# Kernel optimization log

Hardware: AMD Instinct MI355X
Metric: run time of the kernel (lower is better)

## Reference

```python
import jax, jax.numpy as jnp
import numpy as np

HIDDEN = 4096
NUM_HEADS = 32
NUM_KV_HEADS = 8
HEAD_DIM = 128
ROPE_THETA = 10000.0


def setup_inputs() -> dict:
    key = jax.random.key(0)
    ks = jax.random.split(key, 5)
    B, N = 2, 2048
    s = 0.02
    return {
        "hidden_states": jax.random.normal(ks[0], (B, N, HIDDEN), dtype=jnp.float32),
        "positions": jnp.tile(jnp.arange(N, dtype=jnp.int32)[None, :], (B, 1)),
        "Wq": jax.random.normal(ks[1], (HIDDEN, NUM_HEADS * HEAD_DIM), dtype=jnp.float32) * s,
        "Wk": jax.random.normal(ks[2], (HIDDEN, NUM_KV_HEADS * HEAD_DIM), dtype=jnp.float32) * s,
        "Wv": jax.random.normal(ks[3], (HIDDEN, NUM_KV_HEADS * HEAD_DIM), dtype=jnp.float32) * s,
        "Wo": jax.random.normal(ks[4], (NUM_HEADS * HEAD_DIM, HIDDEN), dtype=jnp.float32) * s,
    }


def _rotate_half(x):
    half = x.shape[-1] // 2
    return jnp.concatenate([-x[..., half:], x[..., :half]], axis=-1)


def reference(hidden_states, positions, Wq, Wk, Wv, Wo):
    B, N, _ = hidden_states.shape
    H, KVH, D = NUM_HEADS, NUM_KV_HEADS, HEAD_DIM
    rep = H // KVH

    # projections
    q = (hidden_states @ Wq).reshape(B, N, H, D).transpose(0, 2, 1, 3)     # [B,H,N,D]
    k = (hidden_states @ Wk).reshape(B, N, KVH, D).transpose(0, 2, 1, 3)   # [B,KVH,N,D]
    v = (hidden_states @ Wv).reshape(B, N, KVH, D).transpose(0, 2, 1, 3)   # [B,KVH,N,D]

    # rotary embedding
    inv_freq = 1.0 / (ROPE_THETA ** (jnp.arange(0, D, 2, dtype=jnp.float32) / D))
    freqs = positions.astype(jnp.float32)[..., None] * inv_freq            # [B,N,D/2]
    emb = jnp.concatenate([freqs, freqs], axis=-1)                          # [B,N,D]
    cos = jnp.cos(emb)[:, None, :, :]                                       # [B,1,N,D]
    sin = jnp.sin(emb)[:, None, :, :]
    q = q * cos + _rotate_half(q) * sin
    k = k * cos + _rotate_half(k) * sin

    # GQA attention without materializing repeated k/v:
    # group q heads by kv head (repeat_interleave => q head h uses kv group h//rep)
    qg = q.reshape(B, KVH, rep, N, D)
    scale = 1.0 / jnp.sqrt(jnp.asarray(D, dtype=q.dtype))
    scores = jnp.einsum('bgrnd,bgmd->bgrnm', qg, k) * scale                 # [B,KVH,rep,N,N]
    causal = jnp.tril(jnp.ones((N, N), dtype=bool))
    scores = jnp.where(causal, scores, jnp.finfo(scores.dtype).min)
    attn = jax.nn.softmax(scores, axis=-1)
    out = jnp.einsum('bgrnm,bgmd->bgrnd', attn, v)                          # [B,KVH,rep,N,D]
    out = out.reshape(B, H, N, D).transpose(0, 2, 1, 3).reshape(B, N, H * D)
    return out @ Wo
```

## Files before the change

### kernel.cpp

```cpp
#include <hip/hip_runtime.h>
#include <hip/hip_bf16.h>

typedef __bf16 bf16_t;
typedef float  f32x4  __attribute__((ext_vector_type(4)));
typedef bf16_t bf16x4 __attribute__((ext_vector_type(4)));
typedef bf16_t bf16x8 __attribute__((ext_vector_type(8)));

#define MFMA16(a, b, c) __builtin_amdgcn_mfma_f32_16x16x32_bf16((a), (b), (c), 0, 0, 0)

#define GLOAD_LDS16(g, l)                                                              \
  __builtin_amdgcn_global_load_lds((const __attribute__((address_space(1))) void*)(g), \
                                   (__attribute__((address_space(3))) void*)(l), 16, 0, 0)

#define BARRIER    __builtin_amdgcn_s_barrier()
#define WAIT_LGKM0 asm volatile("s_waitcnt lgkmcnt(0)" ::: "memory")
#define WAIT_VM4   asm volatile("s_waitcnt vmcnt(4)" ::: "memory")
#define WAIT_VM6   asm volatile("s_waitcnt vmcnt(6)" ::: "memory")
#define WAIT_VM0   asm volatile("s_waitcnt vmcnt(0)" ::: "memory")

__global__ __launch_bounds__(256) void cvt_bf16(const float* __restrict__ in,
                                                bf16_t* __restrict__ out, int n4) {
  int stride = gridDim.x * blockDim.x;
  for (int i = blockIdx.x * blockDim.x + threadIdx.x; i < n4; i += stride) {
    f32x4 v = ((const f32x4*)in)[i];
    bf16x4 o;
#pragma unroll
    for (int j = 0; j < 4; ++j) o[j] = (bf16_t)v[j];
    ((bf16x4*)out)[i] = o;
  }
}

__global__ __launch_bounds__(256) void transpose_cvt(const float* __restrict__ in,
                                                     bf16_t* __restrict__ out,
                                                     int R, int C) {
  __shared__ float t[64][65];
  int tr0 = blockIdx.y * 64, tc0 = blockIdx.x * 64;
  int tx = threadIdx.x & 15, ty = threadIdx.x >> 4;
#pragma unroll
  for (int i = 0; i < 4; ++i) {
    f32x4 v = *(const f32x4*)(in + (size_t)(tr0 + ty + 16 * i) * C + tc0 + tx * 4);
#pragma unroll
    for (int j = 0; j < 4; ++j) t[ty + 16 * i][tx * 4 + j] = v[j];
  }
  __syncthreads();
#pragma unroll
  for (int i = 0; i < 4; ++i) {
    bf16x4 o4;
#pragma unroll
    for (int j = 0; j < 4; ++j) o4[j] = (bf16_t)t[tx * 4 + j][ty + 16 * i];
    *(bf16x4*)(out + (size_t)(tc0 + ty + 16 * i) * R + tr0 + tx * 4) = o4;
  }
}

#define LDA(buf)                                                                          \
  {                                                                                       \
    const int sb_ = (((buf)*2 + (wr >> 1)) * 128 + (wr & 1) * 64) * 64;                   \
    _Pragma("unroll") for (int mf = 0; mf < 4; ++mf) {                                    \
      int row_ = mf * 16 + ci;                                                            \
      _Pragma("unroll") for (int ks = 0; ks < 2; ++ks)                                    \
          a[mf][ks] = *(const bf16x8*)&lds[sb_ + row_ * 64 +                              \
                                           ((ks * 32 + g * 8) ^ ((ci & 7) << 3))];       \
    }                                                                                     \
  }

#define LDB(buf, nf0, arr)                                                                \
  {                                                                                       \
    const int sb_ = 32768 + ((buf)*2 + wc) * 8192;                                        \
    _Pragma("unroll") for (int j = 0; j < 2; ++j) {                                       \
      int row_ = ((nf0) + j) * 16 + ci;                                                   \
      _Pragma("unroll") for (int ks = 0; ks < 2; ++ks)                                    \
          arr[j][ks] = *(const bf16x8*)&lds[sb_ + row_ * 64 +                             \
                                            ((ks * 32 + g * 8) ^ ((ci & 7) << 3))];      \
    }                                                                                     \
  }

#define MM(arr, NFP)                                                                      \
  {                                                                                       \
    __builtin_amdgcn_s_setprio(1);                                                        \
    _Pragma("unroll") for (int mf = 0; mf < 4; ++mf)                                      \
        _Pragma("unroll") for (int j = 0; j < 2; ++j)                                     \
            _Pragma("unroll") for (int ks = 0; ks < 2; ++ks)                              \
                acc[mf][(NFP) + j] =                                                      \
        MFMA16(a[mf][ks], arr[j][ks], acc[mf][(NFP) + j]);                                \
    __builtin_amdgcn_s_setprio(0);                                                        \
  }

template <int WRITE_BF16>
__global__ __launch_bounds__(512) void gemm8(const bf16_t* __restrict__ A,
                                             const bf16_t* __restrict__ Bt,
                                             void* __restrict__ Cv,
                                             int M, int N, int K, int ntn) {
  __shared__ alignas(16) bf16_t lds[65536];
  (void)M;
  const int tid = threadIdx.x;
  const int lane = tid & 63, w = tid >> 6;
  const int wr = w >> 1, wc = w & 1;
  const int g = lane >> 4, ci = lane & 15;
  const int cpx = gridDim.x >> 3;
  const int wg = ((int)blockIdx.x & 7) * cpx + ((int)blockIdx.x >> 3);
  const int m0 = (wg / ntn) * 256, n0 = (wg % ntn) * 256;
  const int ksw = ((lane & 7) ^ (lane >> 3)) << 3;

  auto stage = [&](const bf16_t* src, int ldsbase) {
#pragma unroll
    for (int j = 0; j < 2; ++j)
      GLOAD_LDS16(src + (size_t)(j * 64 + w * 8 + (lane >> 3)) * K + ksw,
                  (char*)&lds[ldsbase + (j * 64 + w * 8) * 64]);
  };

  bf16x8 a[4][2], b0[2][2], b1[2][2];
  f32x4 acc[4][8];
#pragma unroll
  for (int mf = 0; mf < 4; ++mf)
#pragma unroll
    for (int nf = 0; nf < 8; ++nf) acc[mf][nf] = f32x4{0.f, 0.f, 0.f, 0.f};

  stage(A + (size_t)m0 * K, 0);
  stage(A + (size_t)(m0 + 128) * K, 8192);
  stage(Bt + (size_t)n0 * K, 32768);
  stage(Bt + (size_t)(n0 + 128) * K, 40960);
  WAIT_VM4;
  stage(A + (size_t)m0 * K + 64, 16384);
  stage(A + (size_t)(m0 + 128) * K + 64, 24576);
  stage(Bt + (size_t)n0 * K + 64, 49152);
  WAIT_VM6;
  BARRIER;

  const int NT2 = K >> 7;
  for (int i = 0; i < NT2; ++i) {
    const int keb = i << 7;
    int e2 = keb + 128;
    if (e2 > K - 64) e2 = K - 64;
    int o2 = keb + 192;
    if (o2 > K - 64) o2 = K - 64;
    LDA(0) LDB(0, 0, b0) LDB(0, 2, b1)
    stage(Bt + (size_t)(n0 + 128) * K + keb + 64, 57344);
    BARRIER; WAIT_LGKM0;
    MM(b0, 0)
    BARRIER;
    LDB(0, 4, b0)
    stage(A + (size_t)m0 * K + e2, 0);
    BARRIER; WAIT_LGKM0;
    MM(b1, 2)
    BARRIER;
    LDB(0, 6, b1)
    stage(A + (size_t)(m0 + 128) * K + e2, 8192);
    BARRIER; WAIT_LGKM0;
    MM(b0, 4)
    BARRIER;
    stage(Bt + (size_t)n0 * K + e2, 32768);
    BARRIER; WAIT_LGKM0;
    MM(b1, 6)
    WAIT_VM6;
    BARRIER;
    LDA(1) LDB(1, 0, b0) LDB(1, 2, b1)
    stage(Bt + (size_t)(n0 + 128) * K + e2, 40960);
    BARRIER; WAIT_LGKM0;
    MM(b0, 0)
    BARRIER;
    LDB(1, 4, b0)
    stage(A + (size_t)m0 * K + o2, 16384);
    BARRIER; WAIT_LGKM0;
    MM(b1, 2)
    BARRIER;
    LDB(1, 6, b1)
    stage(A + (size_t)(m0 + 128) * K + o2, 24576);
    BARRIER; WAIT_LGKM0;
    MM(b0, 4)
    BARRIER;
    stage(Bt + (size_t)n0 * K + o2, 49152);
    BARRIER; WAIT_LGKM0;
    MM(b1, 6)
    WAIT_VM6;
    BARRIER;
  }
  WAIT_VM0;

#pragma unroll
  for (int mf = 0; mf < 4; ++mf) {
#pragma unroll
    for (int nf = 0; nf < 8; ++nf) {
      int grow = m0 + wr * 64 + mf * 16 + g * 4;
      int gcol = n0 + wc * 128 + nf * 16 + ci;
#pragma unroll
      for (int r = 0; r < 4; ++r) {
        if (WRITE_BF16)
          ((bf16_t*)Cv)[(size_t)(grow + r) * N + gcol] = (bf16_t)acc[mf][nf][r];
        else
          ((float*)Cv)[(size_t)(grow + r) * N + gcol] = acc[mf][nf][r];
      }
    }
  }
}

__global__ __launch_bounds__(256) void rope_pack(const bf16_t* __restrict__ QKV,
                                                 const int* __restrict__ pos,
                                                 bf16_t* __restrict__ Qr,
                                                 bf16_t* __restrict__ Kr,
                                                 bf16_t* __restrict__ Vr) {
  int unit = blockIdx.x * 4 + (threadIdx.x >> 6);
  int lane = threadIdx.x & 63;
  int token = unit / 48, slot = unit % 48;
  int b = token >> 11, n = token & 2047;
  const bf16_t* base = QKV + (size_t)token * 6144;
  if (slot < 40) {
    float p = (float)pos[token];
    float inv = exp2f(-(float)lane * 0.20762050593045702f);
    float ang = p * inv;
    float sn, cs;
    sincosf(ang, &sn, &cs);
    const bf16_t* src;
    bf16_t* dst;
    if (slot < 32) {
      src = base + slot * 128;
      dst = Qr + ((size_t)(b * 32 + slot) * 2048 + n) * 128;
    } else {
      int kvh = slot - 32;
      src = base + 4096 + kvh * 128;
      dst = Kr + ((size_t)(b * 8 + kvh) * 2048 + n) * 128;
    }
    float x0 = (float)src[lane], x1 = (float)src[lane + 64];
    dst[lane] = (bf16_t)(x0 * cs - x1 * sn);
    dst[lane + 64] = (bf16_t)(x1 * cs + x0 * sn);
  } else {
    int kvh = slot - 40;
    const bf16_t* src = base + 5120 + kvh * 128;
    bf16_t* dst = Vr + ((size_t)(b * 8 + kvh) * 2048 + n) * 128;
    dst[lane] = src[lane];
    dst[lane + 64] = src[lane + 64];
  }
}

__global__ __launch_bounds__(512) void attn_kernel(const bf16_t* __restrict__ Q,
                                                   const bf16_t* __restrict__ K,
                                                   const bf16_t* __restrict__ V,
                                                   bf16_t* __restrict__ O) {
  const float scale = 0.08838834764831845f;
  __shared__ alignas(16) bf16_t Kl[64 * 128];
  __shared__ alignas(16) bf16_t Vt[128 * 64];
  __shared__ alignas(16) bf16_t Pl[8][32 * 64];
  const int tid = threadIdx.x;
  const int lane = tid & 63, w = tid >> 6;
  const int g = lane >> 4, ci = lane & 15;
  const int hb = blockIdx.y;
  const int b = hb >> 5, h = hb & 31, kvh = h >> 2;
  const int p = blockIdx.x;
  const int qtB = 15 - p;
  const int qr[2] = {p * 128 + w * 16, qtB * 128 + w * 16};
  const bf16_t* Qh = Q + (size_t)hb * 2048 * 128;
  const bf16_t* Kh = K + (size_t)(b * 8 + kvh) * 2048 * 128;
  const bf16_t* Vh = V + (size_t)(b * 8 + kvh) * 2048 * 128;

  bf16x8 bq[2][4];
#pragma unroll
  for (int qb = 0; qb < 2; ++qb)
#pragma unroll
    for (int ks = 0; ks < 4; ++ks)
      bq[qb][ks] = *(const bf16x8*)(Qh + (size_t)(qr[qb] + ci) * 128 + ks * 32 + g * 8);

  f32x4 o[2][8];
#pragma unroll
  for (int qb = 0; qb < 2; ++qb)
#pragma unroll
    for (int nb = 0; nb < 8; ++nb) o[qb][nb] = f32x4{0.f, 0.f, 0.f, 0.f};
  float mrow[2] = {-1e30f, -1e30f};
  float lrow[2] = {0.f, 0.f};

  const int nt = (qtB + 1) * 2;
  for (int t = 0; t < nt; ++t) {
    const int kv0 = t * 64;
    __syncthreads();
#pragma unroll
    for (int i = 0; i < 2; ++i) {
      int c = tid + i * 512;
      int row = c >> 4, kc = (c & 15) * 8;
      bf16x8 kx = *(const bf16x8*)(Kh + (size_t)(kv0 + row) * 128 + kc);
      int sw = ((row ^ (row >> 3)) & 7) << 4;
      *(bf16x8*)((char*)Kl + row * 256 + ((kc * 2) ^ sw)) = kx;
    }
    {
      int kq = tid >> 5, dq = tid & 31;
      bf16x4 rv[4];
#pragma unroll
      for (int rr = 0; rr < 4; ++rr)
        rv[rr] = *(const bf16x4*)(Vh + (size_t)(kv0 + kq * 4 + rr) * 128 + dq * 4);
#pragma unroll
      for (int jj = 0; jj < 4; ++jj) {
        int d = dq * 4 + jj;
        bf16x4 cv;
#pragma unroll
        for (int rr = 0; rr < 4; ++rr) cv[rr] = rv[rr][jj];
        int sw = ((d ^ (d >> 3)) & 7) << 4;
        *(bf16x4*)((char*)Vt + d * 128 + ((kq * 8) ^ sw)) = cv;
      }
    }
    __syncthreads();

    bool act[2] = {kv0 <= qr[0] + 15, kv0 <= qr[1] + 15};
#pragma unroll
    for (int qb = 0; qb < 2; ++qb) {
      if (!act[qb]) continue;
      f32x4 st[4];
#pragma unroll
      for (int kvb = 0; kvb < 4; ++kvb) st[kvb] = f32x4{0.f, 0.f, 0.f, 0.f};
      __builtin_amdgcn_s_setprio(1);
#pragma unroll
      for (int kvb = 0; kvb < 4; ++kvb) {
        int row = kvb * 16 + ci;
        int sw = ((row ^ (row >> 3)) & 7) << 4;
#pragma unroll
        for (int ks = 0; ks < 4; ++ks) {
          bf16x8 ak = *(const bf16x8*)((char*)Kl + row * 256 + ((ks * 64 + g * 16) ^ sw));
          st[kvb] = MFMA16(ak, bq[qb][ks], st[kvb]);
        }
      }
      __builtin_amdgcn_s_setprio(0);
      const int q = qr[qb] + ci;
      const bool needmask = (kv0 + 63 > qr[qb]);
      float pv[16];
      float pm = -1e30f;
#pragma unroll
      for (int kvb = 0; kvb < 4; ++kvb)
#pragma unroll
        for (int r = 0; r < 4; ++r) {
          float v = st[kvb][r] * scale;
          if (needmask && (kv0 + kvb * 16 + 4 * g + r > q)) v = -1e30f;
          pv[kvb * 4 + r] = v;
          pm = fmaxf(pm, v);
        }
      pm = fmaxf(pm, __shfl_xor(pm, 16));
      pm = fmaxf(pm, __shfl_xor(pm, 32));
      float mnew = fmaxf(mrow[qb], pm);
      float fs = __expf(mrow[qb] - mnew);
      mrow[qb] = mnew;
      float ps = 0.f;
#pragma unroll
      for (int e = 0; e < 16; ++e) {
        pv[e] = __expf(pv[e] - mnew);
        ps += pv[e];
      }
      ps += __shfl_xor(ps, 16);
      ps += __shfl_xor(ps, 32);
      lrow[qb] = lrow[qb] * fs + ps;
      int prow = qb * 16 + ci;
      int swp = ((prow ^ (prow >> 3)) & 7) << 4;
#pragma unroll
      for (int kvb = 0; kvb < 4; ++kvb) {
        bf16x4 pk;
#pragma unroll
        for (int r = 0; r < 4; ++r) pk[r] = (bf16_t)pv[kvb * 4 + r];
        *(bf16x4*)((char*)&Pl[w][0] + prow * 128 + (((kvb * 16 + 4 * g) * 2) ^ swp)) = pk;
      }
      float fo[4];
#pragma unroll
      for (int r = 0; r < 4; ++r) fo[r] = __shfl(fs, 4 * g + r);
#pragma unroll
      for (int nb = 0; nb < 8; ++nb)
#pragma unroll
        for (int r = 0; r < 4; ++r) o[qb][nb][r] *= fo[r];
    }
    bf16x8 pa[2][2];
#pragma unroll
    for (int qb = 0; qb < 2; ++qb) {
      if (!act[qb]) continue;
      int prow = qb * 16 + ci;
      int swp = ((prow ^ (prow >> 3)) & 7) << 4;
#pragma unroll
      for (int ks = 0; ks < 2; ++ks)
        pa[qb][ks] = *(const bf16x8*)((char*)&Pl[w][0] + prow * 128 + ((ks * 64 + g * 16) ^ swp));
    }
    __builtin_amdgcn_s_setprio(1);
#pragma unroll
    for (int nb = 0; nb < 8; ++nb) {
      int d = nb * 16 + ci;
      int sw = ((d ^ (d >> 3)) & 7) << 4;
      bf16x8 bv0 = *(const bf16x8*)((char*)Vt + d * 128 + ((g * 16) ^ sw));
      bf16x8 bv1 = *(const bf16x8*)((char*)Vt + d * 128 + ((64 + g * 16) ^ sw));
#pragma unroll
      for (int qb = 0; qb < 2; ++qb) {
        if (!act[qb]) continue;
        o[qb][nb] = MFMA16(pa[qb][0], bv0, o[qb][nb]);
        o[qb][nb] = MFMA16(pa[qb][1], bv1, o[qb][nb]);
      }
    }
    __builtin_amdgcn_s_setprio(0);
  }
#pragma unroll
  for (int qb = 0; qb < 2; ++qb) {
    float linv = 1.0f / lrow[qb];
    float lv[4];
#pragma unroll
    for (int r = 0; r < 4; ++r) lv[r] = __shfl(linv, 4 * g + r);
#pragma unroll
    for (int r = 0; r < 4; ++r) {
      int n = qr[qb] + 4 * g + r;
      bf16_t* op = O + (size_t)(b * 2048 + n) * 4096 + h * 128;
#pragma unroll
      for (int nb = 0; nb < 8; ++nb) op[nb * 16 + ci] = (bf16_t)(o[qb][nb][r] * lv[r]);
    }
  }
}

extern "C" void kernel_launch(void* const* d_in, const int* in_sizes, int n_in,
                              void* d_out, int out_size, void* d_ws, size_t ws_size,
                              hipStream_t stream) {
  (void)in_sizes; (void)n_in; (void)out_size; (void)ws_size;
  const float* X = (const float*)d_in[0];
  const int* pos = (const int*)d_in[1];
  const float* Wq = (const float*)d_in[2];
  const float* Wk = (const float*)d_in[3];
  const float* Wv = (const float*)d_in[4];
  const float* Wo = (const float*)d_in[5];
  float* out = (float*)d_out;

  char* w = (char*)d_ws;
  auto carve = [&](size_t bytes) {
    void* p = (void*)w;
    w += (bytes + 255) & ~(size_t)255;
    return p;
  };
  const size_t T = 4096;
  bf16_t* Xbf    = (bf16_t*)carve(T * 4096 * 2);
  bf16_t* WqkvT  = (bf16_t*)carve(6144ull * 4096 * 2);
  bf16_t* WoT    = (bf16_t*)carve(4096ull * 4096 * 2);
  bf16_t* QKVraw = (bf16_t*)carve(T * 6144 * 2);
  bf16_t* Qr     = (bf16_t*)carve(T * 4096 * 2);
  bf16_t* Kr     = (bf16_t*)carve(T * 1024 * 2);
  bf16_t* Vr     = (bf16_t*)carve(T * 1024 * 2);
  bf16_t* Obf    = (bf16_t*)carve(T * 4096 * 2);

  cvt_bf16<<<2048, 256, 0, stream>>>(X, Xbf, (int)(T * 4096 / 4));
  transpose_cvt<<<dim3(64, 64), 256, 0, stream>>>(Wq, WqkvT, 4096, 4096);
  transpose_cvt<<<dim3(16, 64), 256, 0, stream>>>(Wk, WqkvT + 4096ull * 4096, 4096, 1024);
  transpose_cvt<<<dim3(16, 64), 256, 0, stream>>>(Wv, WqkvT + 5120ull * 4096, 4096, 1024);
  transpose_cvt<<<dim3(64, 64), 256, 0, stream>>>(Wo, WoT, 4096, 4096);

  gemm8<1><<<384, 512, 0, stream>>>(Xbf, WqkvT, QKVraw, 4096, 6144, 4096, 24);

  rope_pack<<<(int)(T * 48 / 4), 256, 0, stream>>>(QKVraw, pos, Qr, Kr, Vr);

  attn_kernel<<<dim3(8, 64), 512, 0, stream>>>(Qr, Kr, Vr, Obf);

  gemm8<0><<<256, 512, 0, stream>>>(Obf, WoT, out, 4096, 4096, 4096, 16);
}
```

Before: 589.9 us.

## Rework GEMM warp tiling to 2x4 with 128x64 warp tiles; add lazy softmax rescale

The bf16 GEMM changes its 8-wave layout from 4x2 warps with 64x128 tiles to 2x4 warps with 128x64 tiles. Each warp now loads its full B fragment once per k-slice and streams A in quarters, which reorders the LDS staging schedule and the wait counts. The attention kernel adds a FlashAttention-style lazy rescale: the running max, and with it the output and row-sum rescaling, is only updated when some lane's new max exceeds the old one by more than 8. This trades a little numerical headroom in the exponentials for fewer shuffles and multiplies. The reworked pipeline schedule carries some risk of stalls or hazards.

Result: no change. 582.8 us (-1.2%).

```diff
diff --git a/kernel.cpp b/kernel.cpp
--- a/kernel.cpp
+++ b/kernel.cpp
@@ -14,8 +14,8 @@
 
 #define BARRIER    __builtin_amdgcn_s_barrier()
 #define WAIT_LGKM0 asm volatile("s_waitcnt lgkmcnt(0)" ::: "memory")
+#define WAIT_LGKM8 asm volatile("s_waitcnt lgkmcnt(8)" ::: "memory")
 #define WAIT_VM4   asm volatile("s_waitcnt vmcnt(4)" ::: "memory")
-#define WAIT_VM6   asm volatile("s_waitcnt vmcnt(6)" ::: "memory")
 #define WAIT_VM0   asm volatile("s_waitcnt vmcnt(0)" ::: "memory")
 
 __global__ __launch_bounds__(256) void cvt_bf16(const float* __restrict__ in,
@@ -52,136 +52,142 @@
   }
 }
 
-#define LDA(buf)                                                                          \
-  {                                                                                       \
-    const int sb_ = (((buf)*2 + (wr >> 1)) * 128 + (wr & 1) * 64) * 64;                   \
-    _Pragma("unroll") for (int mf = 0; mf < 4; ++mf) {                                    \
-      int row_ = mf * 16 + ci;                                                            \
-      _Pragma("unroll") for (int ks = 0; ks < 2; ++ks)                                    \
-          a[mf][ks] = *(const bf16x8*)&lds[sb_ + row_ * 64 +                              \
-                                           ((ks * 32 + g * 8) ^ ((ci & 7) << 3))];       \
-    }                                                                                     \
-  }
-
-#define LDB(buf, nf0, arr)                                                                \
-  {                                                                                       \
-    const int sb_ = 32768 + ((buf)*2 + wc) * 8192;                                        \
-    _Pragma("unroll") for (int j = 0; j < 2; ++j) {                                       \
-      int row_ = ((nf0) + j) * 16 + ci;                                                   \
-      _Pragma("unroll") for (int ks = 0; ks < 2; ++ks)                                    \
-          arr[j][ks] = *(const bf16x8*)&lds[sb_ + row_ * 64 +                             \
-                                            ((ks * 32 + g * 8) ^ ((ci & 7) << 3))];      \
-    }                                                                                     \
-  }
-
-#define MM(arr, NFP)                                                                      \
-  {                                                                                       \
-    __builtin_amdgcn_s_setprio(1);                                                        \
-    _Pragma("unroll") for (int mf = 0; mf < 4; ++mf)                                      \
-        _Pragma("unroll") for (int j = 0; j < 2; ++j)                                     \
-            _Pragma("unroll") for (int ks = 0; ks < 2; ++ks)                              \
-                acc[mf][(NFP) + j] =                                                      \
-        MFMA16(a[mf][ks], arr[j][ks], acc[mf][(NFP) + j]);                                \
-    __builtin_amdgcn_s_setprio(0);                                                        \
+#define LDB8(bf)                                                                         \
+  {                                                                                      \
+    const int sb_ = bBase0 + (bf)*16384;                                                 \
+    _Pragma("unroll") for (int nf = 0; nf < 4; ++nf) {                                   \
+      int row_ = brow0 + nf * 16 + ci;                                                   \
+      _Pragma("unroll") for (int ks = 0; ks < 2; ++ks)                                   \
+          b[nf][ks] = *(const bf16x8*)&lds[sb_ + row_ * 64 + ((ks * 32 + g * 8) ^ co)];  \
+    }                                                                                    \
+  }
+
+#define LDA4(bf, q)                                                                      \
+  {                                                                                      \
+    const int sb_ = aBase0 + (bf)*16384;                                                 \
+    _Pragma("unroll") for (int j = 0; j < 2; ++j) {                                      \
+      int row_ = ((q)*2 + j) * 16 + ci;                                                  \
+      _Pragma("unroll") for (int ks = 0; ks < 2; ++ks)                                   \
+          a[j][ks] = *(const bf16x8*)&lds[sb_ + row_ * 64 + ((ks * 32 + g * 8) ^ co)];   \
+    }                                                                                    \
+  }
+
+#define MMQ(q)                                                                           \
+  {                                                                                      \
+    __builtin_amdgcn_s_setprio(1);                                                       \
+    _Pragma("unroll") for (int j = 0; j < 2; ++j)                                        \
+        _Pragma("unroll") for (int nf = 0; nf < 4; ++nf)                                 \
+            _Pragma("unroll") for (int ks = 0; ks < 2; ++ks)                             \
+                acc[(q)*2 + j][nf] = MFMA16(a[j][ks], b[nf][ks], acc[(q)*2 + j][nf]);    \
+    __builtin_amdgcn_s_setprio(0);                                                       \
   }
 
 template <int WRITE_BF16>
 __global__ __launch_bounds__(512) void gemm8(const bf16_t* __restrict__ A,
                                              const bf16_t* __restrict__ Bt,
                                              void* __restrict__ Cv,
-                                             int M, int N, int K, int ntn) {
+                                             int N, int K, int ntn) {
   __shared__ alignas(16) bf16_t lds[65536];
-  (void)M;
   const int tid = threadIdx.x;
   const int lane = tid & 63, w = tid >> 6;
-  const int wr = w >> 1, wc = w & 1;
+  const int wr = w >> 2, wc = w & 3;
   const int g = lane >> 4, ci = lane & 15;
   const int cpx = gridDim.x >> 3;
   const int wg = ((int)blockIdx.x & 7) * cpx + ((int)blockIdx.x >> 3);
   const int m0 = (wg / ntn) * 256, n0 = (wg % ntn) * 256;
   const int ksw = ((lane & 7) ^ (lane >> 3)) << 3;
-
-  auto stage = [&](const bf16_t* src, int ldsbase) {
+  const int aBase0 = wr * 8192;
+  const int bBase0 = 32768 + (wc >> 1) * 8192;
+  const int brow0 = (wc & 1) * 64;
+  const int co = (ci & 7) << 3;
+
+  const bf16_t* As[2] = {A + (size_t)m0 * K, A + (size_t)(m0 + 128) * K};
+  const bf16_t* Bs[2] = {Bt + (size_t)n0 * K, Bt + (size_t)(n0 + 128) * K};
+
+  auto stage = [&](const bf16_t* src, int kk, int ldsbase) {
 #pragma unroll
     for (int j = 0; j < 2; ++j)
-      GLOAD_LDS16(src + (size_t)(j * 64 + w * 8 + (lane >> 3)) * K + ksw,
+      GLOAD_LDS16(src + (size_t)(j * 64 + w * 8 + (lane >> 3)) * K + kk + ksw,
                   (char*)&lds[ldsbase + (j * 64 + w * 8) * 64]);
   };
 
-  bf16x8 a[4][2], b0[2][2], b1[2][2];
-  f32x4 acc[4][8];
-#pragma unroll
-  for (int mf = 0; mf < 4; ++mf)
-#pragma unroll
-    for (int nf = 0; nf < 8; ++nf) acc[mf][nf] = f32x4{0.f, 0.f, 0.f, 0.f};
-
-  stage(A + (size_t)m0 * K, 0);
-  stage(A + (size_t)(m0 + 128) * K, 8192);
-  stage(Bt + (size_t)n0 * K, 32768);
-  stage(Bt + (size_t)(n0 + 128) * K, 40960);
+  bf16x8 a[2][2], b[4][2];
+  f32x4 acc[8][4];
+#pragma unroll
+  for (int mf = 0; mf < 8; ++mf)
+#pragma unroll
+    for (int nf = 0; nf < 4; ++nf) acc[mf][nf] = f32x4{0.f, 0.f, 0.f, 0.f};
+
+  stage(As[0], 0, 0);
+  stage(As[1], 0, 8192);
+  stage(Bs[0], 0, 32768);
+  stage(Bs[1], 0, 40960);
+  stage(Bs[0], 64, 49152);
+  stage(Bs[1], 64, 57344);
   WAIT_VM4;
-  stage(A + (size_t)m0 * K + 64, 16384);
-  stage(A + (size_t)(m0 + 128) * K + 64, 24576);
-  stage(Bt + (size_t)n0 * K + 64, 49152);
-  WAIT_VM6;
   BARRIER;
 
   const int NT2 = K >> 7;
   for (int i = 0; i < NT2; ++i) {
     const int keb = i << 7;
+    const int kA1 = keb + 64;
     int e2 = keb + 128;
     if (e2 > K - 64) e2 = K - 64;
     int o2 = keb + 192;
     if (o2 > K - 64) o2 = K - 64;
-    LDA(0) LDB(0, 0, b0) LDB(0, 2, b1)
-    stage(Bt + (size_t)(n0 + 128) * K + keb + 64, 57344);
-    BARRIER; WAIT_LGKM0;
-    MM(b0, 0)
-    BARRIER;
-    LDB(0, 4, b0)
-    stage(A + (size_t)m0 * K + e2, 0);
-    BARRIER; WAIT_LGKM0;
-    MM(b1, 2)
-    BARRIER;
-    LDB(0, 6, b1)
-    stage(A + (size_t)(m0 + 128) * K + e2, 8192);
-    BARRIER; WAIT_LGKM0;
-    MM(b0, 4)
-    BARRIER;
-    stage(Bt + (size_t)n0 * K + e2, 32768);
-    BARRIER; WAIT_LGKM0;
-    MM(b1, 6)
-    WAIT_VM6;
-    BARRIER;
-    LDA(1) LDB(1, 0, b0) LDB(1, 2, b1)
-    stage(Bt + (size_t)(n0 + 128) * K + e2, 40960);
-    BARRIER; WAIT_LGKM0;
-    MM(b0, 0)
-    BARRIER;
-    LDB(1, 4, b0)
-    stage(A + (size_t)m0 * K + o2, 16384);
-    BARRIER; WAIT_LGKM0;
-    MM(b1, 2)
-    BARRIER;
-    LDB(1, 6, b1)
-    stage(A + (size_t)(m0 + 128) * K + o2, 24576);
-    BARRIER; WAIT_LGKM0;
-    MM(b0, 4)
-    BARRIER;
-    stage(Bt + (size_t)n0 * K + o2, 49152);
-    BARRIER; WAIT_LGKM0;
-    MM(b1, 6)
-    WAIT_VM6;
+    LDA4(0, 0) LDB8(0)
+    stage(As[0], kA1, 16384);
+    WAIT_LGKM8;
+    BARRIER; WAIT_LGKM0;
+    MMQ(0)
+    BARRIER;
+    LDA4(0, 1)
+    stage(As[1], kA1, 24576);
+    BARRIER; WAIT_LGKM0;
+    MMQ(1)
+    BARRIER;
+    LDA4(0, 2)
+    stage(Bs[0], e2, 32768);
+    BARRIER; WAIT_LGKM0;
+    MMQ(2)
+    BARRIER;
+    LDA4(0, 3)
+    stage(Bs[1], e2, 40960);
+    BARRIER; WAIT_LGKM0;
+    MMQ(3)
+    WAIT_VM4;
+    BARRIER;
+    LDA4(1, 0) LDB8(1)
+    stage(As[0], e2, 0);
+    WAIT_LGKM8;
+    BARRIER; WAIT_LGKM0;
+    MMQ(0)
+    BARRIER;
+    LDA4(1, 1)
+    stage(As[1], e2, 8192);
+    BARRIER; WAIT_LGKM0;
+    MMQ(1)
+    BARRIER;
+    LDA4(1, 2)
+    stage(Bs[0], o2, 49152);
+    BARRIER; WAIT_LGKM0;
+    MMQ(2)
+    BARRIER;
+    LDA4(1, 3)
+    stage(Bs[1], o2, 57344);
+    BARRIER; WAIT_LGKM0;
+    MMQ(3)
+    WAIT_VM4;
     BARRIER;
   }
   WAIT_VM0;
 
 #pragma unroll
-  for (int mf = 0; mf < 4; ++mf) {
-#pragma unroll
-    for (int nf = 0; nf < 8; ++nf) {
-      int grow = m0 + wr * 64 + mf * 16 + g * 4;
-      int gcol = n0 + wc * 128 + nf * 16 + ci;
+  for (int mf = 0; mf < 8; ++mf) {
+#pragma unroll
+    for (int nf = 0; nf < 4; ++nf) {
+      int grow = m0 + wr * 128 + mf * 16 + g * 4;
+      int gcol = n0 + wc * 64 + nf * 16 + ci;
 #pragma unroll
       for (int r = 0; r < 4; ++r) {
         if (WRITE_BF16)
@@ -330,9 +336,15 @@
         }
       pm = fmaxf(pm, __shfl_xor(pm, 16));
       pm = fmaxf(pm, __shfl_xor(pm, 32));
-      float mnew = fmaxf(mrow[qb], pm);
-      float fs = __expf(mrow[qb] - mnew);
-      mrow[qb] = mnew;
+      const bool nskip = !__all((int)(pm <= mrow[qb] + 8.0f));
+      const float mold = mrow[qb];
+      float mnew = mold;
+      float fs = 1.0f;
+      if (nskip) {
+        mnew = fmaxf(mold, pm);
+        fs = __expf(mold - mnew);
+        mrow[qb] = mnew;
+      }
       float ps = 0.f;
 #pragma unroll
       for (int e = 0; e < 16; ++e) {
@@ -341,7 +353,7 @@
       }
       ps += __shfl_xor(ps, 16);
       ps += __shfl_xor(ps, 32);
-      lrow[qb] = lrow[qb] * fs + ps;
+      lrow[qb] = (nskip ? lrow[qb] * fs : lrow[qb]) + ps;
       int prow = qb * 16 + ci;
       int swp = ((prow ^ (prow >> 3)) & 7) << 4;
 #pragma unroll
@@ -351,13 +363,15 @@
         for (int r = 0; r < 4; ++r) pk[r] = (bf16_t)pv[kvb * 4 + r];
         *(bf16x4*)((char*)&Pl[w][0] + prow * 128 + (((kvb * 16 + 4 * g) * 2) ^ swp)) = pk;
       }
-      float fo[4];
-#pragma unroll
-      for (int r = 0; r < 4; ++r) fo[r] = __shfl(fs, 4 * g + r);
-#pragma unroll
-      for (int nb = 0; nb < 8; ++nb)
-#pragma unroll
-        for (int r = 0; r < 4; ++r) o[qb][nb][r] *= fo[r];
+      if (nskip) {
+        float fo[4];
+#pragma unroll
+        for (int r = 0; r < 4; ++r) fo[r] = __shfl(fs, 4 * g + r);
+#pragma unroll
+        for (int nb = 0; nb < 8; ++nb)
+#pragma unroll
+          for (int r = 0; r < 4; ++r) o[qb][nb][r] *= fo[r];
+      }
     }
     bf16x8 pa[2][2];
 #pragma unroll
@@ -435,11 +449,11 @@
   transpose_cvt<<<dim3(16, 64), 256, 0, stream>>>(Wv, WqkvT + 5120ull * 4096, 4096, 1024);
   transpose_cvt<<<dim3(64, 64), 256, 0, stream>>>(Wo, WoT, 4096, 4096);
 
-  gemm8<1><<<384, 512, 0, stream>>>(Xbf, WqkvT, QKVraw, 4096, 6144, 4096, 24);
+  gemm8<1><<<384, 512, 0, stream>>>(Xbf, WqkvT, QKVraw, 6144, 4096, 24);
 
   rope_pack<<<(int)(T * 48 / 4), 256, 0, stream>>>(QKVraw, pos, Qr, Kr, Vr);
 
   attn_kernel<<<dim3(8, 64), 512, 0, stream>>>(Qr, Kr, Vr, Obf);
 
-  gemm8<0><<<256, 512, 0, stream>>>(Obf, WoT, out, 4096, 4096, 4096, 16);
-}
+  gemm8<0><<<256, 512, 0, stream>>>(Obf, WoT, out, 4096, 4096, 16);
+}
```
